# Optimization experiments

Measured on AMD Instinct MI355X. Metric: run time of the kernel, lower is better.

The kernel has to match this reference:

```python
import jax, jax.numpy as jnp
import numpy as np

WIN_SIZE = 256           # GlobalConfig.win_size (assumed)
NFFT = 2 * WIN_SIZE      # 512 -> NFREQ = 257 rfft bins
HOP = WIN_SIZE
NFREQ = WIN_SIZE + 1
K = 3                    # all kernel sizes in the model
EPS = 1e-5


def _stft(x):
    # x: (B, S) -> (B, T, F, 2) real view of complex STFT (hann window, no center)
    B, S = x.shape
    T = (S - NFFT) // HOP + 1
    n = jnp.arange(NFFT)
    win = 0.5 - 0.5 * jnp.cos(2.0 * jnp.pi * n / NFFT)
    idx = jnp.arange(T)[:, None] * HOP + n[None, :]
    frames = x[:, idx] * win                       # (B, T, NFFT)
    spec = jnp.fft.rfft(frames, axis=-1)           # (B, T, F) complex
    return jnp.stack([spec.real, spec.imag], axis=-1).astype(x.dtype)


def _td_layer(x, W, b, same):
    # time-distributed conv over the frequency axis. x: (B,T,F,Cin), W: (k,Cin,Cout)
    k = W.shape[0]
    if same:
        x = jnp.pad(x, ((0, 0), (0, 0), (k // 2, k - 1 - k // 2), (0, 0)))
    Fout = x.shape[2] - k + 1
    xs = jnp.stack([x[:, :, i:i + Fout] for i in range(k)], axis=0)  # (k,B,T,Fout,Cin)
    return jnp.einsum('kbtfc,kco->btfo', xs, W) + b


def _td_block(x, W1, b1, W2, b2):
    h = jax.nn.relu(_td_layer(x, W1, b1, True))
    return _td_layer(h, W2, b2, True)


def _layer(x, g, beta, dw, W1, b1, W2, b2):
    # LayerNorm over (F, C), causal depthwise conv over T, TD pointwise block, ReLU
    B, T, F, C = x.shape
    mu = x.mean(axis=(-2, -1), keepdims=True)
    var = x.var(axis=(-2, -1), keepdims=True)
    xn = (x - mu) * jax.lax.rsqrt(var + EPS) * g + beta
    h = xn.reshape(B, T, F * C)
    hp = jnp.pad(h, ((0, 0), (K - 1, 0), (0, 0)))   # causal left-pad on time
    y = sum(hp[:, i:i + T, :] * dw[:, i] for i in range(K))  # (B,T,F*C) depthwise
    y = y.reshape(B, T, F, C)
    return jax.nn.relu(_td_block(y, W1, b1, W2, b2))


def setup_inputs() -> dict:
    key = jax.random.key(0)
    ks = iter(jax.random.split(key, 40))
    def rn(shape, s=0.05):
        return (jax.random.normal(next(ks), shape) * s).astype(jnp.float32)
    F = NFREQ
    d = {}
    d['x'] = jax.random.normal(next(ks), (8, 262144), dtype=jnp.float32)
    d['l0_W1'] = rn((3, 2, 4)); d['l0_b1'] = jnp.zeros((4,), jnp.float32)
    d['l0_W2'] = rn((3, 4, 8)); d['l0_b2'] = jnp.zeros((8,), jnp.float32)
    for name, cin in (('l1', 8), ('l2', 16), ('l3', 24)):
        d[name + '_g'] = jnp.ones((F, cin), jnp.float32)
        d[name + '_bn'] = jnp.zeros((F, cin), jnp.float32)
        d[name + '_dw'] = rn((F * cin, 3), 0.3)
        d[name + '_W1'] = rn((3, cin, 8)); d[name + '_b1'] = jnp.zeros((8,), jnp.float32)
        d[name + '_W2'] = rn((3, 8, 8)); d[name + '_b2'] = jnp.zeros((8,), jnp.float32)
    d['fc1_W'] = rn((3, 32, 1)); d['fc1_b'] = jnp.zeros((1,), jnp.float32)
    d['fc2_W'] = rn((F - 2, 1)); d['fc2_b'] = jnp.zeros((1,), jnp.float32)
    return d


def reference(x, l0_W1, l0_b1, l0_W2, l0_b2,
              l1_g, l1_bn, l1_dw, l1_W1, l1_b1, l1_W2, l1_b2,
              l2_g, l2_bn, l2_dw, l2_W1, l2_b1, l2_W2, l2_b2,
              l3_g, l3_bn, l3_dw, l3_W1, l3_b1, l3_W2, l3_b2,
              fc1_W, fc1_b, fc2_W, fc2_b):
    s = _stft(x)                                            # (B,T,F,2)
    h = jax.nn.relu(_td_block(s, l0_W1, l0_b1, l0_W2, l0_b2))  # (B,T,F,8)
    h = jnp.concatenate([h, _layer(h, l1_g, l1_bn, l1_dw, l1_W1, l1_b1, l1_W2, l1_b2)], axis=3)
    h = jnp.concatenate([h, _layer(h, l2_g, l2_bn, l2_dw, l2_W1, l2_b1, l2_W2, l2_b2)], axis=3)
    h = jnp.concatenate([h, _layer(h, l3_g, l3_bn, l3_dw, l3_W1, l3_b1, l3_W2, l3_b2)], axis=3)
    h = jax.nn.relu(_td_layer(h, fc1_W, fc1_b, False))[..., 0]  # (B,T,F-2)
    out = jax.nn.sigmoid(h @ fc2_W + fc2_b)                 # (B,T,1)
    return out[..., 0]                                      # (B,T)
```

## Files before the change

### kernel.cpp

```cpp
#include <hip/hip_runtime.h>
#include <hip/hip_fp16.h>

namespace {

constexpr int BATCH = 8;
constexpr int SLEN  = 262144;
constexpr int TT    = 1023;
constexpr int NF    = 257;
constexpr int NCH   = 24;
constexpr int NBT   = BATCH * TT;
constexpr int FRS   = NCH * NF;
constexpr float EPS = 1e-5f;

__device__ inline int div257(int e) { return (e * 65282) >> 24; }

__global__ __launch_bounds__(256) void stft_l0_kernel(
    const float* __restrict__ x,
    const float* __restrict__ W1g, const float* __restrict__ b1g,
    const float* __restrict__ W2g, const float* __restrict__ b2g,
    __half* __restrict__ H, float* __restrict__ stats0)
{
  __shared__ float  xw[512];
  __shared__ float2 ab[256];
  __shared__ float  sre[NF + 2];
  __shared__ float  sim[NF + 2];
  __shared__ float  h1[4][NF + 2];
  __shared__ float  wW1[24], wb1[4], wW2[96], wb2[8];
  __shared__ float  red[8];

  const int tid = threadIdx.x;
  const int bt  = blockIdx.x;
  const int b   = bt / TT;
  const int t   = bt - b * TT;
  const float* xp = x + (size_t)b * SLEN + (size_t)t * 256;

  if (tid < 24) wW1[tid] = W1g[tid];
  if (tid < 4)  wb1[tid] = b1g[tid];
  if (tid < 96) wW2[tid] = W2g[tid];
  if (tid < 8)  wb2[tid] = b2g[tid];

  const float STEP = 6.283185307179586f / 512.0f;
  for (int n = tid; n < 512; n += 256) {
    float sv, cv;
    sincosf(STEP * (float)n, &sv, &cv);
    xw[n] = xp[n] * (0.5f - 0.5f * cv);
  }
  __syncthreads();

  if (tid == 0) ab[0] = make_float2(0.f, 0.f);
  if (tid >= 1) {
    float u = xw[tid], v = xw[512 - tid];
    ab[tid] = make_float2(u + v, u - v);
  }
  __syncthreads();

  const float x0 = xw[0], x256 = xw[256];

  {
    const int k = tid;
    float s1, c1;
    sincosf(STEP * (float)k, &s1, &c1);
    const float c2 = fmaf(c1, c1, -s1 * s1), s2 = 2.f * c1 * s1;
    const float c3 = fmaf(c2, c1, -s2 * s1), s3 = fmaf(c2, s1, s2 * c1);
    const float c4 = fmaf(c2, c2, -s2 * s2), s4 = 2.f * c2 * s2;
    float cA = 1.f, sA = 0.f;
    float cB = c1,  sB = s1;
    float cC = c2,  sC = s2;
    float cD = c3,  sD = s3;
    float re = x0 + ((k & 1) ? -x256 : x256);
    float im = 0.f;
    for (int m = 0; m < 64; ++m) {
      const float2 p0 = ab[4*m],     p1 = ab[4*m + 1];
      const float2 p2 = ab[4*m + 2], p3 = ab[4*m + 3];
      re = fmaf(p0.x, cA, re); im = fmaf(-p0.y, sA, im);
      re = fmaf(p1.x, cB, re); im = fmaf(-p1.y, sB, im);
      re = fmaf(p2.x, cC, re); im = fmaf(-p2.y, sC, im);
      re = fmaf(p3.x, cD, re); im = fmaf(-p3.y, sD, im);
      float t0;
      t0 = fmaf(cA, c4, -sA * s4); sA = fmaf(cA, s4, sA * c4); cA = t0;
      t0 = fmaf(cB, c4, -sB * s4); sB = fmaf(cB, s4, sB * c4); cB = t0;
      t0 = fmaf(cC, c4, -sC * s4); sC = fmaf(cC, s4, sC * c4); cC = t0;
      t0 = fmaf(cD, c4, -sD * s4); sD = fmaf(cD, s4, sD * c4); cD = t0;
    }
    sre[1 + k] = re;
    sim[1 + k] = im;
  }

  {
    float ps = 0.f;
    if (tid >= 1) ps = (tid & 1) ? -ab[tid].x : ab[tid].x;
    #pragma unroll
    for (int off = 32; off > 0; off >>= 1) ps += __shfl_down(ps, off, 64);
    if ((tid & 63) == 0) red[tid >> 6] = ps;
    __syncthreads();
    if (tid == 0) {
      sre[257] = x0 + x256 + red[0] + red[1] + red[2] + red[3];
      sim[257] = 0.f;
      sre[0] = 0.f; sim[0] = 0.f; sre[258] = 0.f; sim[258] = 0.f;
    }
  }
  __syncthreads();

  for (int f = tid; f < NF; f += 256) {
    float acc[4] = {wb1[0], wb1[1], wb1[2], wb1[3]};
    #pragma unroll
    for (int i = 0; i < 3; ++i) {
      float vr = sre[f + i], vi = sim[f + i];
      #pragma unroll
      for (int c = 0; c < 4; ++c)
        acc[c] = fmaf(vr, wW1[(i*2+0)*4 + c], fmaf(vi, wW1[(i*2+1)*4 + c], acc[c]));
    }
    #pragma unroll
    for (int c = 0; c < 4; ++c) h1[c][f + 1] = fmaxf(acc[c], 0.f);
  }
  if (tid < 4) { h1[tid][0] = 0.f; h1[tid][NF + 1] = 0.f; }
  __syncthreads();

  const size_t obase = (size_t)bt * FRS;
  float ps1 = 0.f, ps2 = 0.f;
  for (int f = tid; f < NF; f += 256) {
    float acc[8];
    #pragma unroll
    for (int c = 0; c < 8; ++c) acc[c] = wb2[c];
    #pragma unroll
    for (int i = 0; i < 3; ++i)
      #pragma unroll
      for (int c4 = 0; c4 < 4; ++c4) {
        float hv = h1[c4][f + i];
        #pragma unroll
        for (int c = 0; c < 8; ++c)
          acc[c] = fmaf(hv, wW2[(i*4+c4)*8 + c], acc[c]);
      }
    #pragma unroll
    for (int c = 0; c < 8; ++c) {
      const __half hv = __float2half(fmaxf(acc[c], 0.f));
      H[obase + (size_t)c * NF + f] = hv;
      const float v = __half2float(hv);
      ps1 += v;
      ps2 = fmaf(v, v, ps2);
    }
  }
  #pragma unroll
  for (int off = 32; off > 0; off >>= 1) {
    ps1 += __shfl_down(ps1, off, 64);
    ps2 += __shfl_down(ps2, off, 64);
  }
  if ((tid & 63) == 0) { red[(tid >> 6) * 2] = ps1; red[(tid >> 6) * 2 + 1] = ps2; }
  __syncthreads();
  if (tid == 0) {
    stats0[bt * 2]     = red[0] + red[2] + red[4] + red[6];
    stats0[bt * 2 + 1] = red[1] + red[3] + red[5] + red[7];
  }
}

template<int CIN>
__global__ __launch_bounds__(256) void fold_tbl(
    const float* __restrict__ g, const float* __restrict__ bn,
    const float* __restrict__ dw, __half* __restrict__ dst)
{
  constexpr int NEL = CIN * NF;
  const int idx = blockIdx.x * 256 + threadIdx.x;
  if (idx >= NEL) return;
  const int c = div257(idx), f = idx - c * 257;
  const int s = f * CIN + c;
  const float gv = g[s], bv = bn[s];
  const float d0 = dw[s * 3], d1 = dw[s * 3 + 1], d2 = dw[s * 3 + 2];
  dst[idx]           = __float2half(gv * d0);
  dst[NEL + idx]     = __float2half(gv * d1);
  dst[2 * NEL + idx] = __float2half(gv * d2);
  dst[3 * NEL + idx] = __float2half(bv * (d0 + d1 + d2));
  dst[4 * NEL + idx] = __float2half(bv * (d1 + d2));
  dst[5 * NEL + idx] = __float2half(bv * d2);
}

template<int CIN, bool HEAD>
__global__ __launch_bounds__(256, 4) void layer_bt(
    const __half* __restrict__ H, __half* __restrict__ Hout,
    const float* __restrict__ st0, const float* __restrict__ st1,
    const float* __restrict__ st2, float* __restrict__ stats_out,
    const __half* __restrict__ tbl,
    const float* __restrict__ W1g, const float* __restrict__ b1g,
    const float* __restrict__ W2g, const float* __restrict__ b2g,
    const float* __restrict__ fc1W, const float* __restrict__ fc1b,
    const float* __restrict__ fc2W, const float* __restrict__ fc2b,
    float* __restrict__ out)
{
  constexpr int NEL   = CIN * NF;
  constexpr int NP2   = NEL / 2;
  constexpr int NPER2 = (NP2 + 255) / 256;
  constexpr int TAIL2 = NP2 - 256 * (NPER2 - 1);

  __shared__ float y[CIN * 259];
  __shared__ float h1[8 * 259];
  __shared__ float wW1[3 * CIN * 8], wb1[8], wW2[192], wb2[8];
  __shared__ float red[8];
  __shared__ float wfc1[HEAD ? 96 : 1];

  const int tid = threadIdx.x;
  const int bt  = blockIdx.x;
  const int b   = bt / TT;
  const int t   = bt - b * TT;

  for (int i = tid; i < 3 * CIN * 8; i += 256) wW1[i] = W1g[i];
  if (tid < 192) wW2[tid] = W2g[tid];
  if (tid < 8) { wb1[tid] = b1g[tid]; wb2[tid] = b2g[tid]; }
  if (tid < CIN) { y[tid * 259] = 0.f; y[tid * 259 + 258] = 0.f; }
  if (tid < 8)   { h1[tid * 259] = 0.f; h1[tid * 259 + 258] = 0.f; }
  if constexpr (HEAD) { if (tid < 96) wfc1[tid] = fc1W[tid]; }

  float mu0 = 0.f, rs0 = 0.f, mu1 = 0.f, rs1 = 0.f, mu2, rs2;
  {
    const float inv = 1.0f / (float)NEL;
    float s1 = st0[bt * 2], s2v = st0[bt * 2 + 1];
    if constexpr (CIN >= 16) { s1 += st1[bt * 2]; s2v += st1[bt * 2 + 1]; }
    if constexpr (CIN >= 24) { s1 += st2[bt * 2]; s2v += st2[bt * 2 + 1]; }
    mu2 = s1 * inv; rs2 = rsqrtf(s2v * inv - mu2 * mu2 + EPS);
    if (t >= 1) {
      const int fb = bt - 1;
      float a = st0[fb * 2], c = st0[fb * 2 + 1];
      if constexpr (CIN >= 16) { a += st1[fb * 2]; c += st1[fb * 2 + 1]; }
      if constexpr (CIN >= 24) { a += st2[fb * 2]; c += st2[fb * 2 + 1]; }
      mu1 = a * inv; rs1 = rsqrtf(c * inv - mu1 * mu1 + EPS);
    }
    if (t >= 2) {
      const int fb = bt - 2;
      float a = st0[fb * 2], c = st0[fb * 2 + 1];
      if constexpr (CIN >= 16) { a += st1[fb * 2]; c += st1[fb * 2 + 1]; }
      if constexpr (CIN >= 24) { a += st2[fb * 2]; c += st2[fb * 2 + 1]; }
      mu0 = a * inv; rs0 = rsqrtf(c * inv - mu0 * mu0 + EPS);
    }
  }

  const int base = b * TT;
  const __half2* f2p = (const __half2*)(H + (size_t)bt * FRS);
  const __half2* f1p = (const __half2*)(H + (size_t)max(bt - 1, base) * FRS);
  const __half2* f0p = (const __half2*)(H + (size_t)max(bt - 2, base) * FRS);
  const __half2* P0p = (const __half2*)tbl;
  const __half2* P1p = (const __half2*)(tbl + NEL);
  const __half2* P2p = (const __half2*)(tbl + 2 * NEL);
  const int qsel = (t >= 2) ? 0 : (t == 1 ? 1 : 2);
  const __half2* Qp  = (const __half2*)(tbl + (3 + qsel) * NEL);

  #pragma unroll
  for (int j = 0; j < NPER2; ++j) {
    const bool act = (j < NPER2 - 1) || (tid < TAIL2);
    if (act) {
      const int p  = tid + 256 * j;
      const int e0 = 2 * p;
      const int c0 = div257(e0);
      const int fi = e0 - c0 * 257;
      const float2 xa = __half22float2(f0p[p]);
      const float2 xb = __half22float2(f1p[p]);
      const float2 xc = __half22float2(f2p[p]);
      const float2 pa = __half22float2(P0p[p]);
      const float2 pb = __half22float2(P1p[p]);
      const float2 pc = __half22float2(P2p[p]);
      const float2 qq = __half22float2(Qp[p]);
      const float y0 = fmaf((xa.x - mu0) * rs0, pa.x,
                       fmaf((xb.x - mu1) * rs1, pb.x,
                       fmaf((xc.x - mu2) * rs2, pc.x, qq.x)));
      const float y1 = fmaf((xa.y - mu0) * rs0, pa.y,
                       fmaf((xb.y - mu1) * rs1, pb.y,
                       fmaf((xc.y - mu2) * rs2, pc.y, qq.y)));
      const int a0 = c0 * 259 + 1 + fi;
      y[a0] = y0;
      y[a0 + ((fi == 256) ? 3 : 1)] = y1;
    }
  }
  __syncthreads();

  {
    const int f = tid;
    float acc[8];
    #pragma unroll
    for (int c = 0; c < 8; ++c) acc[c] = wb1[c];
    #pragma unroll
    for (int i = 0; i < 3; ++i)
      for (int cin = 0; cin < CIN; ++cin) {
        const float yv = y[cin * 259 + f + i];
        #pragma unroll
        for (int c = 0; c < 8; ++c)
          acc[c] = fmaf(yv, wW1[(i * CIN + cin) * 8 + c], acc[c]);
      }
    #pragma unroll
    for (int c = 0; c < 8; ++c) h1[c * 259 + 1 + f] = fmaxf(acc[c], 0.f);
  }
  if (tid < 8) {
    float a = wb1[tid];
    #pragma unroll
    for (int i = 0; i < 3; ++i)
      for (int cin = 0; cin < CIN; ++cin)
        a = fmaf(y[cin * 259 + 256 + i], wW1[(i * CIN + cin) * 8 + tid], a);
    h1[tid * 259 + 257] = fmaxf(a, 0.f);
  }
  __syncthreads();

  float* out2 = y;
  float ps1 = 0.f, ps2 = 0.f;
  {
    const int f = tid;
    float o2[8];
    #pragma unroll
    for (int c = 0; c < 8; ++c) o2[c] = wb2[c];
    #pragma unroll
    for (int i = 0; i < 3; ++i)
      #pragma unroll
      for (int c8 = 0; c8 < 8; ++c8) {
        const float hv = h1[c8 * 259 + f + i];
        #pragma unroll
        for (int c = 0; c < 8; ++c)
          o2[c] = fmaf(hv, wW2[(i * 8 + c8) * 8 + c], o2[c]);
      }
    if constexpr (!HEAD) {
      const size_t ob = (size_t)bt * FRS + (size_t)CIN * NF;
      #pragma unroll
      for (int c = 0; c < 8; ++c) {
        const __half hv = __float2half(fmaxf(o2[c], 0.f));
        Hout[ob + (size_t)c * NF + f] = hv;
        const float v = __half2float(hv);
        ps1 += v;
        ps2 = fmaf(v, v, ps2);
      }
    } else {
      #pragma unroll
      for (int c = 0; c < 8; ++c) out2[c * 257 + f] = fmaxf(o2[c], 0.f);
    }
  }
  if (tid >= 8 && tid < 16) {
    const int c8 = tid - 8;
    float a = wb2[c8];
    #pragma unroll
    for (int i = 0; i < 3; ++i)
      #pragma unroll
      for (int cp = 0; cp < 8; ++cp)
        a = fmaf(h1[cp * 259 + 256 + i], wW2[(i * 8 + cp) * 8 + c8], a);
    if constexpr (!HEAD) {
      const size_t ob = (size_t)bt * FRS + (size_t)CIN * NF;
      const __half hv = __float2half(fmaxf(a, 0.f));
      Hout[ob + (size_t)c8 * NF + 256] = hv;
      const float v = __half2float(hv);
      ps1 += v;
      ps2 = fmaf(v, v, ps2);
    } else {
      out2[c8 * 257 + 256] = fmaxf(a, 0.f);
    }
  }

  if constexpr (!HEAD) {
    #pragma unroll
    for (int off = 32; off > 0; off >>= 1) {
      ps1 += __shfl_down(ps1, off, 64);
      ps2 += __shfl_down(ps2, off, 64);
    }
    if ((tid & 63) == 0) { red[(tid >> 6) * 2] = ps1; red[(tid >> 6) * 2 + 1] = ps2; }
    __syncthreads();
    if (tid == 0) {
      stats_out[bt * 2]     = red[0] + red[2] + red[4] + red[6];
      stats_out[bt * 2 + 1] = red[1] + red[3] + red[5] + red[7];
    }
  } else {
    __syncthreads();
    float part = 0.f;
    if (tid < NF - 2) {
      const __half* xg = (const __half*)f2p;
      float acc = fc1b[0];
      #pragma unroll
      for (int i = 0; i < 3; ++i) {
        for (int c = 0; c < 24; ++c)
          acc = fmaf(__half2float(xg[c * 257 + tid + i]), wfc1[i * 32 + c], acc);
        #pragma unroll
        for (int c8 = 0; c8 < 8; ++c8)
          acc = fmaf(out2[c8 * 257 + tid + i], wfc1[i * 32 + 24 + c8], acc);
      }
      part = fmaxf(acc, 0.f) * fc2W[tid];
    }
    #pragma unroll
    for (int off = 32; off > 0; off >>= 1) part += __shfl_down(part, off, 64);
    if ((tid & 63) == 0) red[tid >> 6] = part;
    __syncthreads();
    if (tid == 0) {
      const float tot = red[0] + red[1] + red[2] + red[3] + fc2b[0];
      out[bt] = 1.0f / (1.0f + expf(-tot));
    }
  }
}

}

extern "C" void kernel_launch(void* const* d_in, const int* in_sizes, int n_in,
                              void* d_out, int out_size, void* d_ws, size_t ws_size,
                              hipStream_t stream) {
  (void)in_sizes; (void)n_in; (void)out_size; (void)ws_size;
  const float* x = (const float*)d_in[0];
  float* out = (float*)d_out;
  char*  wsb = (char*)d_ws;

  __half* H   = (__half*)wsb;
  char* p = wsb + (size_t)NBT * FRS * sizeof(__half);
  float* st0  = (float*)p; p += 2 * NBT * sizeof(float);
  float* st1  = (float*)p; p += 2 * NBT * sizeof(float);
  float* st2  = (float*)p; p += 2 * NBT * sizeof(float);
  __half* tbl1 = (__half*)p; p += 6 * (8  * NF) * sizeof(__half);
  __half* tbl2 = (__half*)p; p += 6 * (16 * NF) * sizeof(__half);
  __half* tbl3 = (__half*)p;

  dim3 blk(256);

  fold_tbl<8><<<dim3((8 * NF + 255) / 256), blk, 0, stream>>>(
      (const float*)d_in[5], (const float*)d_in[6], (const float*)d_in[7], tbl1);
  fold_tbl<16><<<dim3((16 * NF + 255) / 256), blk, 0, stream>>>(
      (const float*)d_in[12], (const float*)d_in[13], (const float*)d_in[14], tbl2);
  fold_tbl<24><<<dim3((24 * NF + 255) / 256), blk, 0, stream>>>(
      (const float*)d_in[19], (const float*)d_in[20], (const float*)d_in[21], tbl3);

  stft_l0_kernel<<<dim3(NBT), blk, 0, stream>>>(
      x, (const float*)d_in[1], (const float*)d_in[2],
      (const float*)d_in[3], (const float*)d_in[4], H, st0);

  layer_bt<8, false><<<dim3(NBT), blk, 0, stream>>>(
      H, H, st0, nullptr, nullptr, st1, tbl1,
      (const float*)d_in[8], (const float*)d_in[9],
      (const float*)d_in[10], (const float*)d_in[11],
      nullptr, nullptr, nullptr, nullptr, nullptr);

  layer_bt<16, false><<<dim3(NBT), blk, 0, stream>>>(
      H, H, st0, st1, nullptr, st2, tbl2,
      (const float*)d_in[15], (const float*)d_in[16],
      (const float*)d_in[17], (const float*)d_in[18],
      nullptr, nullptr, nullptr, nullptr, nullptr);

  layer_bt<24, true><<<dim3(NBT), blk, 0, stream>>>(
      H, nullptr, st0, st1, st2, nullptr, tbl3,
      (const float*)d_in[22], (const float*)d_in[23],
      (const float*)d_in[24], (const float*)d_in[25],
      (const float*)d_in[26], (const float*)d_in[27],
      (const float*)d_in[28], (const float*)d_in[29],
      out);
}
```

Measured before the change: 448.8 us.

## Exploit real-input DFT symmetry, store layer scratch in half, raise occupancy

The STFT DFT loop now runs on 128 threads and uses even/odd partial sums to produce bins k and 256-k together, with float4 shared loads. The other 128 threads compute the Nyquist/middle bin with a wave reduction. The layer kernels keep their y/h1 shared scratch in fp16 and raise launch bounds to 8 blocks per CU. This cuts DFT arithmetic and LDS footprint to allow higher occupancy, at the cost of extra fp16 rounding in intermediates and possible register pressure from the tighter bounds.

```diff
diff --git a/kernel.cpp b/kernel.cpp
--- a/kernel.cpp
+++ b/kernel.cpp
@@ -14,14 +14,14 @@
 
 __device__ inline int div257(int e) { return (e * 65282) >> 24; }
 
-__global__ __launch_bounds__(256) void stft_l0_kernel(
+__global__ __launch_bounds__(256, 8) void stft_l0_kernel(
     const float* __restrict__ x,
     const float* __restrict__ W1g, const float* __restrict__ b1g,
     const float* __restrict__ W2g, const float* __restrict__ b2g,
     __half* __restrict__ H, float* __restrict__ stats0)
 {
   __shared__ float  xw[512];
-  __shared__ float2 ab[256];
+  __shared__ __align__(16) float2 ab[256];
   __shared__ float  sre[NF + 2];
   __shared__ float  sim[NF + 2];
   __shared__ float  h1[4][NF + 2];
@@ -56,7 +56,7 @@
 
   const float x0 = xw[0], x256 = xw[256];
 
-  {
+  if (tid < 128) {
     const int k = tid;
     float s1, c1;
     sincosf(STEP * (float)k, &s1, &c1);
@@ -67,37 +67,46 @@
     float cB = c1,  sB = s1;
     float cC = c2,  sC = s2;
     float cD = c3,  sD = s3;
-    float re = x0 + ((k & 1) ? -x256 : x256);
-    float im = 0.f;
+    float re_e = 0.f, re_o = 0.f, im_e = 0.f, im_o = 0.f;
+    const float4* ab4 = (const float4*)ab;
     for (int m = 0; m < 64; ++m) {
-      const float2 p0 = ab[4*m],     p1 = ab[4*m + 1];
-      const float2 p2 = ab[4*m + 2], p3 = ab[4*m + 3];
-      re = fmaf(p0.x, cA, re); im = fmaf(-p0.y, sA, im);
-      re = fmaf(p1.x, cB, re); im = fmaf(-p1.y, sB, im);
-      re = fmaf(p2.x, cC, re); im = fmaf(-p2.y, sC, im);
-      re = fmaf(p3.x, cD, re); im = fmaf(-p3.y, sD, im);
+      const float4 q0 = ab4[2 * m];
+      const float4 q1 = ab4[2 * m + 1];
+      re_e = fmaf(q0.x, cA, re_e); im_e = fmaf(q0.y, sA, im_e);
+      re_o = fmaf(q0.z, cB, re_o); im_o = fmaf(q0.w, sB, im_o);
+      re_e = fmaf(q1.x, cC, re_e); im_e = fmaf(q1.y, sC, im_e);
+      re_o = fmaf(q1.z, cD, re_o); im_o = fmaf(q1.w, sD, im_o);
       float t0;
       t0 = fmaf(cA, c4, -sA * s4); sA = fmaf(cA, s4, sA * c4); cA = t0;
       t0 = fmaf(cB, c4, -sB * s4); sB = fmaf(cB, s4, sB * c4); cB = t0;
       t0 = fmaf(cC, c4, -sC * s4); sC = fmaf(cC, s4, sC * c4); cC = t0;
       t0 = fmaf(cD, c4, -sD * s4); sD = fmaf(cD, s4, sD * c4); cD = t0;
     }
-    sre[1 + k] = re;
-    sim[1 + k] = im;
-  }
-
-  {
-    float ps = 0.f;
-    if (tid >= 1) ps = (tid & 1) ? -ab[tid].x : ab[tid].x;
-    #pragma unroll
-    for (int off = 32; off > 0; off >>= 1) ps += __shfl_down(ps, off, 64);
-    if ((tid & 63) == 0) red[tid >> 6] = ps;
-    __syncthreads();
-    if (tid == 0) {
-      sre[257] = x0 + x256 + red[0] + red[1] + red[2] + red[3];
-      sim[257] = 0.f;
-      sre[0] = 0.f; sim[0] = 0.f; sre[258] = 0.f; sim[258] = 0.f;
-    }
+    const float rb = x0 + ((k & 1) ? -x256 : x256);
+    sre[1 + k] = rb + re_e + re_o;
+    sim[1 + k] = -(im_e + im_o);
+    sre[1 + 256 - k] = rb + re_e - re_o;
+    sim[1 + 256 - k] = im_e - im_o;
+  } else {
+    const int m = tid - 128;
+    const float sgn = (m & 1) ? -1.f : 1.f;
+    float tr = ab[2 * m].x * sgn;
+    float ti = -ab[2 * m + 1].y * sgn;
+    #pragma unroll
+    for (int off = 32; off > 0; off >>= 1) {
+      tr += __shfl_down(tr, off, 64);
+      ti += __shfl_down(ti, off, 64);
+    }
+    if ((tid & 63) == 0) {
+      const int w = (tid >> 6) - 2;
+      red[w * 2] = tr; red[w * 2 + 1] = ti;
+    }
+  }
+  __syncthreads();
+  if (tid == 0) {
+    sre[1 + 128] = x0 + x256 + red[0] + red[2];
+    sim[1 + 128] = red[1] + red[3];
+    sre[0] = 0.f; sim[0] = 0.f; sre[258] = 0.f; sim[258] = 0.f;
   }
   __syncthreads();
 
@@ -174,7 +183,7 @@
 }
 
 template<int CIN, bool HEAD>
-__global__ __launch_bounds__(256, 4) void layer_bt(
+__global__ __launch_bounds__(256, 8) void layer_bt(
     const __half* __restrict__ H, __half* __restrict__ Hout,
     const float* __restrict__ st0, const float* __restrict__ st1,
     const float* __restrict__ st2, float* __restrict__ stats_out,
@@ -190,8 +199,8 @@
   constexpr int NPER2 = (NP2 + 255) / 256;
   constexpr int TAIL2 = NP2 - 256 * (NPER2 - 1);
 
-  __shared__ float y[CIN * 259];
-  __shared__ float h1[8 * 259];
+  __shared__ __half y[CIN * 259];
+  __shared__ __half h1[8 * 259];
   __shared__ float wW1[3 * CIN * 8], wb1[8], wW2[192], wb2[8];
   __shared__ float red[8];
   __shared__ float wfc1[HEAD ? 96 : 1];
@@ -201,11 +210,12 @@
   const int b   = bt / TT;
   const int t   = bt - b * TT;
 
+  const __half hz = __float2half(0.f);
   for (int i = tid; i < 3 * CIN * 8; i += 256) wW1[i] = W1g[i];
   if (tid < 192) wW2[tid] = W2g[tid];
   if (tid < 8) { wb1[tid] = b1g[tid]; wb2[tid] = b2g[tid]; }
-  if (tid < CIN) { y[tid * 259] = 0.f; y[tid * 259 + 258] = 0.f; }
-  if (tid < 8)   { h1[tid * 259] = 0.f; h1[tid * 259 + 258] = 0.f; }
+  if (tid < CIN) { y[tid * 259] = hz; y[tid * 259 + 258] = hz; }
+  if (tid < 8)   { h1[tid * 259] = hz; h1[tid * 259 + 258] = hz; }
   if constexpr (HEAD) { if (tid < 96) wfc1[tid] = fc1W[tid]; }
 
   float mu0 = 0.f, rs0 = 0.f, mu1 = 0.f, rs1 = 0.f, mu2, rs2;
@@ -263,8 +273,8 @@
                        fmaf((xb.y - mu1) * rs1, pb.y,
                        fmaf((xc.y - mu2) * rs2, pc.y, qq.y)));
       const int a0 = c0 * 259 + 1 + fi;
-      y[a0] = y0;
-      y[a0 + ((fi == 256) ? 3 : 1)] = y1;
+      y[a0] = __float2half(y0);
+      y[a0 + ((fi == 256) ? 3 : 1)] = __float2half(y1);
     }
   }
   __syncthreads();
@@ -277,25 +287,26 @@
     #pragma unroll
     for (int i = 0; i < 3; ++i)
       for (int cin = 0; cin < CIN; ++cin) {
-        const float yv = y[cin * 259 + f + i];
+        const float yv = __half2float(y[cin * 259 + f + i]);
         #pragma unroll
         for (int c = 0; c < 8; ++c)
           acc[c] = fmaf(yv, wW1[(i * CIN + cin) * 8 + c], acc[c]);
       }
     #pragma unroll
-    for (int c = 0; c < 8; ++c) h1[c * 259 + 1 + f] = fmaxf(acc[c], 0.f);
+    for (int c = 0; c < 8; ++c)
+      h1[c * 259 + 1 + f] = __float2half(fmaxf(acc[c], 0.f));
   }
   if (tid < 8) {
     float a = wb1[tid];
     #pragma unroll
     for (int i = 0; i < 3; ++i)
       for (int cin = 0; cin < CIN; ++cin)
-        a = fmaf(y[cin * 259 + 256 + i], wW1[(i * CIN + cin) * 8 + tid], a);
-    h1[tid * 259 + 257] = fmaxf(a, 0.f);
-  }
-  __syncthreads();
-
-  float* out2 = y;
+        a = fmaf(__half2float(y[cin * 259 + 256 + i]), wW1[(i * CIN + cin) * 8 + tid], a);
+    h1[tid * 259 + 257] = __float2half(fmaxf(a, 0.f));
+  }
+  __syncthreads();
+
+  __half* out2 = y;
   float ps1 = 0.f, ps2 = 0.f;
   {
     const int f = tid;
@@ -306,7 +317,7 @@
     for (int i = 0; i < 3; ++i)
       #pragma unroll
       for (int c8 = 0; c8 < 8; ++c8) {
-        const float hv = h1[c8 * 259 + f + i];
+        const float hv = __half2float(h1[c8 * 259 + f + i]);
         #pragma unroll
         for (int c = 0; c < 8; ++c)
           o2[c] = fmaf(hv, wW2[(i * 8 + c8) * 8 + c], o2[c]);
@@ -323,7 +334,8 @@
       }
     } else {
       #pragma unroll
-      for (int c = 0; c < 8; ++c) out2[c * 257 + f] = fmaxf(o2[c], 0.f);
+      for (int c = 0; c < 8; ++c)
+        out2[c * 257 + f] = __float2half(fmaxf(o2[c], 0.f));
     }
   }
   if (tid >= 8 && tid < 16) {
@@ -333,7 +345,7 @@
     for (int i = 0; i < 3; ++i)
       #pragma unroll
       for (int cp = 0; cp < 8; ++cp)
-        a = fmaf(h1[cp * 259 + 256 + i], wW2[(i * 8 + cp) * 8 + c8], a);
+        a = fmaf(__half2float(h1[cp * 259 + 256 + i]), wW2[(i * 8 + cp) * 8 + c8], a);
     if constexpr (!HEAD) {
       const size_t ob = (size_t)bt * FRS + (size_t)CIN * NF;
       const __half hv = __float2half(fmaxf(a, 0.f));
@@ -342,7 +354,7 @@
       ps1 += v;
       ps2 = fmaf(v, v, ps2);
     } else {
-      out2[c8 * 257 + 256] = fmaxf(a, 0.f);
+      out2[c8 * 257 + 256] = __float2half(fmaxf(a, 0.f));
     }
   }
 
@@ -370,7 +382,7 @@
           acc = fmaf(__half2float(xg[c * 257 + tid + i]), wfc1[i * 32 + c], acc);
         #pragma unroll
         for (int c8 = 0; c8 < 8; ++c8)
-          acc = fmaf(out2[c8 * 257 + tid + i], wfc1[i * 32 + 24 + c8], acc);
+          acc = fmaf(__half2float(out2[c8 * 257 + tid + i]), wfc1[i * 32 + 24 + c8], acc);
       }
       part = fmaxf(acc, 0.f) * fc2W[tid];
     }
```

Result: no change. 442.3 us (-1.4%).
